# Kernel tuning notes

Hardware: AMD Instinct MI355X
Metric: run time of the kernel (lower is better)

Reference implementation:

```python
import jax, jax.numpy as jnp
import numpy as np

T = 1.0        # temperature t from __init__
THRESH = 0.3   # hard-negative margin from forward
B, D, C, P, N = 64, 256, 100000, 8, 32


def setup_inputs():
    key = jax.random.key(0)
    k1, k2, k3, k4, k5, k6, k7 = jax.random.split(key, 7)
    inputs = jax.random.normal(k1, (B, D), jnp.float32)
    V = jax.random.normal(k2, (C, D), jnp.float32) * 0.05  # memory bank (buffer)
    targets = jax.random.randint(k3, (B,), 0, C)
    pos_idx = jax.random.randint(k4, (B, P), 0, B)
    neg_idx = jax.random.randint(k5, (B, N), 0, B)
    pos_mask = jax.random.randint(k6, (B, P), 0, 2).at[:, 0].set(1)  # >=1 positive
    neg_mask = jax.random.randint(k7, (B, N), 0, 2)
    return {"inputs": inputs, "V": V, "targets": targets,
            "pos_idx": pos_idx, "pos_mask": pos_mask,
            "neg_idx": neg_idx, "neg_mask": neg_mask}


def _forward(inputs, V, targets, pos_idx, pos_mask, neg_idx, neg_mask):
    # Exclusive.forward: inputs @ V.T, scaled by t
    logits = (inputs @ V.T) * T                       # [B, C]
    logp = jax.nn.log_softmax(logits, axis=-1)
    bu_loss = -jnp.mean(jnp.take_along_axis(logp, targets[:, None], axis=1))

    # cosine similarity among batch samples
    nrm = jnp.maximum(jnp.linalg.norm(inputs, axis=1, keepdims=True), 1e-12)
    ni = inputs / nrm
    sim = ni @ ni.T                                   # [B, B]

    rows = jnp.arange(B)[:, None]
    # hardest positive: min similarity over valid positive pairs
    psims = sim[rows, pos_idx]                        # [B, P]
    pm = pos_mask.astype(bool)
    hpsims = jnp.min(jnp.where(pm, psims, jnp.inf), axis=1)   # [B]
    hp_loss = jax.nn.softplus(-hpsims)                # BCE-with-logits vs target 1

    # hard negatives: those with sim > (hardest_pos - 0.3)
    nsims = sim[rows, neg_idx]                        # [B, N]
    sel = neg_mask.astype(bool) & (nsims > (hpsims - THRESH)[:, None])
    cnt = jnp.sum(sel, axis=1)
    hn_sum = jnp.sum(jnp.where(sel, jax.nn.softplus(nsims), 0.0), axis=1)
    hn_loss = jnp.where(cnt > 0, hn_sum / jnp.maximum(cnt, 1), 0.0)

    h_loss = jnp.mean(hp_loss + hn_loss)
    return bu_loss + h_loss, logits


def reference(inputs, V, targets, pos_idx, pos_mask, neg_idx, neg_mask):
    return _forward(inputs, V, targets, pos_idx, pos_mask, neg_idx, neg_mask)
```

## Files before the change

kernel.cpp:

```cpp
#include <hip/hip_runtime.h>
#include <hip/hip_bf16.h>
#include <math.h>

#define B_DIM 64
#define D_DIM 256
#define C_DIM 100000
#define P_DIM 8
#define N_DIM 32
#define BLK_COLS 128
#define GBLK 782
#define NCHUNK 8
#define NBANK 64

typedef __attribute__((ext_vector_type(8))) short bf16x8;
typedef __attribute__((ext_vector_type(16))) float f32x16;

__device__ __forceinline__ unsigned short bf16_rn(float f) {
    unsigned int u = __float_as_uint(f);
    unsigned int r = (u + 0x7FFFu + ((u >> 16) & 1u)) >> 16;
    return (unsigned short)r;
}

__device__ __forceinline__ void split_bf16(float x, unsigned short& hi, unsigned short& lo) {
    unsigned int bx = __float_as_uint(x);
    unsigned int hb = bx & 0xFFFF0000u;
    hi = (unsigned short)(hb >> 16);
    lo = bf16_rn(x - __uint_as_float(hb));
}

__device__ __forceinline__ float softplusf(float x) { return log1pf(expf(x)); }

__device__ __forceinline__ short f2bf(float x) {
    __hip_bfloat16 b = __float2bfloat16(x);
    return *reinterpret_cast<short*>(&b);
}

__device__ __forceinline__ void async_copy16(const float* src, float* lds_base) {
    __builtin_amdgcn_global_load_lds(
        (const __attribute__((address_space(1))) unsigned int*)src,
        (__attribute__((address_space(3))) unsigned int*)lds_base,
        16, 0, 0);
}

__global__ __launch_bounds__(512)
void prep_kernel(const float* __restrict__ X,
                 const int* __restrict__ pos_idx, const int* __restrict__ pos_mask,
                 const int* __restrict__ neg_idx, const int* __restrict__ neg_mask,
                 float* __restrict__ wsH, unsigned short* __restrict__ wsA,
                 float* __restrict__ wsQ, float* __restrict__ wsT) {
    __shared__ unsigned short fHi[2048 * 8];
    __shared__ unsigned short fLo[2048 * 8];
    __shared__ float sim[64][64];
    __shared__ float inv[64];
    __shared__ float hp[64];
    __shared__ float contrib[64];
    const int tid = threadIdx.x;
    for (int i = tid; i < NBANK * 64; i += 512) wsQ[i] = 0.0f;
    if (tid < 64) wsT[tid] = 0.0f;
    if (tid < 256) {
        int r = tid >> 2, q = tid & 3;
        const float* row = X + r * D_DIM + q * 64;
        float s = 0.0f;
        #pragma unroll
        for (int i = 0; i < 64; i += 4) {
            float4 v = *(const float4*)(row + i);
            s += v.x * v.x + v.y * v.y + v.z * v.z + v.w * v.w;
        }
        s += __shfl_xor(s, 1);
        s += __shfl_xor(s, 2);
        if (q == 0) inv[r] = 1.0f / fmaxf(sqrtf(s), 1e-12f);
    }
    __syncthreads();
    for (int t = tid; t < 2048; t += 512) {
        int l = t & 63, kg = (t >> 6) & 15, mt = t >> 10;
        int row = mt * 32 + (l & 31);
        int col0 = kg * 16 + 8 * (l >> 5);
        const float* src = X + row * D_DIM + col0;
        float iv = inv[row];
        #pragma unroll
        for (int j = 0; j < 8; ++j) {
            unsigned short h, lo;
            split_bf16(src[j] * iv, h, lo);
            fHi[t * 8 + j] = h;
            fLo[t * 8 + j] = lo;
            wsA[t * 8 + j] = (unsigned short)f2bf(src[j]);
        }
    }
    __syncthreads();
    if ((tid >> 6) < 4) {
        int w = tid >> 6, l = tid & 63;
        int mt = w >> 1, nt = w & 1;
        f32x16 acc;
        #pragma unroll
        for (int i = 0; i < 16; ++i) acc[i] = 0.0f;
        #pragma unroll
        for (int ks = 0; ks < 16; ++ks) {
            const bf16x8 ah = *(const bf16x8*)&fHi[((mt * 16 + ks) * 64 + l) * 8];
            const bf16x8 al = *(const bf16x8*)&fLo[((mt * 16 + ks) * 64 + l) * 8];
            const bf16x8 bh = *(const bf16x8*)&fHi[((nt * 16 + ks) * 64 + l) * 8];
            const bf16x8 bl = *(const bf16x8*)&fLo[((nt * 16 + ks) * 64 + l) * 8];
            acc = __builtin_amdgcn_mfma_f32_32x32x16_bf16(ah, bh, acc, 0, 0, 0);
            acc = __builtin_amdgcn_mfma_f32_32x32x16_bf16(al, bh, acc, 0, 0, 0);
            acc = __builtin_amdgcn_mfma_f32_32x32x16_bf16(ah, bl, acc, 0, 0, 0);
        }
        #pragma unroll
        for (int r = 0; r < 16; ++r) {
            int brow = mt * 32 + (r & 3) + 8 * (r >> 2) + 4 * (l >> 5);
            int bcol = nt * 32 + (l & 31);
            sim[brow][bcol] = acc[r];
        }
    }
    __syncthreads();
    if (tid < 256) {
        int r = tid >> 2, q = tid & 3;
        const float INF = __int_as_float(0x7f800000);
        float m = INF;
        #pragma unroll
        for (int pp = 0; pp < 2; ++pp) {
            int p = q * 2 + pp;
            int j = pos_idx[r * P_DIM + p];
            int msk = pos_mask[r * P_DIM + p];
            float ps = sim[r][j];
            m = fminf(m, msk ? ps : INF);
        }
        m = fminf(m, __shfl_xor(m, 1));
        m = fminf(m, __shfl_xor(m, 2));
        if (q == 0) hp[r] = m;
    }
    __syncthreads();
    if (tid < 256) {
        int r = tid >> 2, q = tid & 3;
        float thr = hp[r] - 0.3f;
        float sum = 0.0f; int cnt = 0;
        #pragma unroll
        for (int nn = 0; nn < 8; ++nn) {
            int n = q * 8 + nn;
            int j = neg_idx[r * N_DIM + n];
            int msk = neg_mask[r * N_DIM + n];
            float ns = sim[r][j];
            if (msk && (ns > thr)) { cnt += 1; sum += softplusf(ns); }
        }
        sum += __shfl_xor(sum, 1); cnt += __shfl_xor(cnt, 1);
        sum += __shfl_xor(sum, 2); cnt += __shfl_xor(cnt, 2);
        if (q == 0) {
            float hn = (cnt > 0) ? (sum / (float)cnt) : 0.0f;
            contrib[r] = softplusf(-hp[r]) + hn;
        }
    }
    __syncthreads();
    if (tid == 0) {
        float s = 0.0f;
        for (int i = 0; i < 64; ++i) s += contrib[i];
        wsH[0] = s * (1.0f / 64.0f);
    }
}

__global__ __launch_bounds__(256)
void logits_kernel(const float* __restrict__ V, const unsigned short* __restrict__ wsA,
                   const int* __restrict__ targets, float* __restrict__ out,
                   float* __restrict__ wsQ, float* __restrict__ wsT) {
    __shared__ float shm[12288];
    __shared__ int tgt[64];
    const int tid = threadIdx.x;
    const int w = tid >> 6, l = tid & 63;
    const int c0 = blockIdx.x * BLK_COLS;
    const int hi = l >> 5;
    if (tid < 64) tgt[tid] = targets[tid];

    #define STAGE(kc, b)                                                        \
        {                                                                       \
            _Pragma("unroll")                                                   \
            for (int j = 0; j < 4; ++j) {                                       \
                int U = (j * 4 + w) * 64 + l;                                   \
                int colL = U >> 3, up = U & 7;                                  \
                int us = up ^ (colL & 7);                                       \
                int cc = c0 + colL; cc = (cc < C_DIM) ? cc : (C_DIM - 1);       \
                const float* src = V + (size_t)cc * D_DIM + (kc) * 32 + us * 4; \
                async_copy16(src, &shm[(b) * 4096 + (j * 4 + w) * 256]);        \
            }                                                                   \
        }

    STAGE(0, 0);
    STAGE(1, 1);

    f32x16 acc0, acc1;
    #pragma unroll
    for (int i = 0; i < 16; ++i) { acc0[i] = 0.0f; acc1[i] = 0.0f; }

    const int colL = w * 32 + (l & 31);
    const int cbase = colL * 32;
    const int cm7 = colL & 7;

    #pragma unroll
    for (int kc = 0; kc < NCHUNK; ++kc) {
        if (kc < NCHUNK - 1) asm volatile("s_waitcnt vmcnt(4)" ::: "memory");
        else                 asm volatile("s_waitcnt vmcnt(0)" ::: "memory");
        __builtin_amdgcn_s_barrier();
        const float* vb = &shm[(kc % 3) * 4096];
        #pragma unroll
        for (int h = 0; h < 2; ++h) {
            const int kg = kc * 2 + h;
            const bf16x8 a0 = *(const bf16x8*)(wsA + ((0 * 16 + kg) * 64 + l) * 8);
            const bf16x8 a1 = *(const bf16x8*)(wsA + ((1 * 16 + kg) * 64 + l) * 8);
            const int u0 = h * 4 + 2 * hi;
            float4 v0 = *(const float4*)&vb[cbase + ((u0    ) ^ cm7) * 4];
            float4 v1 = *(const float4*)&vb[cbase + ((u0 + 1) ^ cm7) * 4];
            bf16x8 vh;
            vh[0] = f2bf(v0.x); vh[1] = f2bf(v0.y); vh[2] = f2bf(v0.z); vh[3] = f2bf(v0.w);
            vh[4] = f2bf(v1.x); vh[5] = f2bf(v1.y); vh[6] = f2bf(v1.z); vh[7] = f2bf(v1.w);
            acc0 = __builtin_amdgcn_mfma_f32_32x32x16_bf16(vh, a0, acc0, 0, 0, 0);
            acc1 = __builtin_amdgcn_mfma_f32_32x32x16_bf16(vh, a1, acc1, 0, 0, 0);
        }
        if (kc < NCHUNK - 2) STAGE(kc + 2, (kc + 2) % 3);
    }
    #undef STAGE
    __syncthreads();

    float* ldsT = &shm[w * 2112];
    float* sred = &shm[8448];
    const int b0 = l & 31, b1 = 32 + (l & 31);
    const int tb0 = tgt[b0], tb1 = tgt[b1];
    float s0 = 0.0f, s1 = 0.0f;
    #pragma unroll
    for (int r = 0; r < 16; ++r) {
        const int cl = (r & 3) + 8 * (r >> 2) + 4 * hi;
        const int c = c0 + w * 32 + cl;
        const float v0 = acc0[r], v1 = acc1[r];
        ldsT[b0 * 33 + cl] = v0;
        ldsT[b1 * 33 + cl] = v1;
        if (c < C_DIM) {
            s0 += expf(v0);
            s1 += expf(v1);
            if (c == tb0) atomicAdd(&wsT[b0], v0);
            if (c == tb1) atomicAdd(&wsT[b1], v1);
        }
    }
    s0 += __shfl_xor(s0, 32);
    s1 += __shfl_xor(s1, 32);
    if (l < 32) { sred[w * 64 + l] = s0; sred[w * 64 + 32 + l] = s1; }
    __syncthreads();
    if (tid < 64) {
        float s = (sred[tid] + sred[64 + tid]) + (sred[128 + tid] + sred[192 + tid]);
        atomicAdd(&wsQ[(blockIdx.x & (NBANK - 1)) * 64 + tid], s);
    }
    const int cg = c0 + w * 32 + (l & 31);
    if (cg < C_DIM) {
        #pragma unroll
        for (int rr = 0; rr < 32; ++rr) {
            const int b = 2 * rr + hi;
            out[1 + (size_t)b * C_DIM + cg] = ldsT[b * 33 + (l & 31)];
        }
    }
}

__global__ __launch_bounds__(64)
void final_kernel(float* __restrict__ out, const float* __restrict__ wsQ,
                  const float* __restrict__ wsT, const float* __restrict__ wsH) {
    int b = threadIdx.x;
    float S = 0.0f;
    #pragma unroll
    for (int k = 0; k < NBANK; ++k) S += wsQ[k * 64 + b];
    float lb = logf(S) - wsT[b];
    #pragma unroll
    for (int m = 1; m <= 32; m <<= 1) lb += __shfl_xor(lb, m);
    if (b == 0) out[0] = lb * (1.0f / 64.0f) + wsH[0];
}

extern "C" void kernel_launch(void* const* d_in, const int* in_sizes, int n_in,
                              void* d_out, int out_size, void* d_ws, size_t ws_size,
                              hipStream_t stream) {
    (void)in_sizes; (void)n_in; (void)out_size; (void)ws_size;
    const float* X        = (const float*)d_in[0];
    const float* V        = (const float*)d_in[1];
    const int*   targets  = (const int*)d_in[2];
    const int*   pos_idx  = (const int*)d_in[3];
    const int*   pos_mask = (const int*)d_in[4];
    const int*   neg_idx  = (const int*)d_in[5];
    const int*   neg_mask = (const int*)d_in[6];
    float* out = (float*)d_out;
    float*          wsH = (float*)d_ws;
    float*          wsQ = (float*)d_ws + 64;
    float*          wsT = (float*)d_ws + 64 + NBANK * 64;
    unsigned short* wsA = (unsigned short*)((char*)d_ws + 32768);

    hipLaunchKernelGGL(prep_kernel, dim3(1), dim3(512), 0, stream,
                       X, pos_idx, pos_mask, neg_idx, neg_mask, wsH, wsA, wsQ, wsT);
    hipLaunchKernelGGL(logits_kernel, dim3(GBLK), dim3(256), 0, stream,
                       V, wsA, targets, out, wsQ, wsT);
    hipLaunchKernelGGL(final_kernel, dim3(1), dim3(64), 0, stream, out, wsQ, wsT, wsH);
}
```

Measured before the change: 53.48 us.

## Fold similarity loss into logits grid and finalize via last-block counter

Replaces the single-block prep kernel with a small parallel bf16 fragment-packing kernel. The cosine-similarity hard-mining loss now runs in an extra block of the logits grid, computing only the needed dot products directly in fp32. The separate final kernel is removed: the last block to finish, detected with an atomic counter, reduces the softmax sums. The logits pipeline also moves to 16-wide K chunks with prefetched A fragments, smaller LDS stages and fewer reduction banks. This saves launch overhead and the serial prep latency, at the cost of fence/atomic completion logic and more barriers per tile.

```diff
diff --git a/kernel.cpp b/kernel.cpp
--- a/kernel.cpp
+++ b/kernel.cpp
@@ -8,25 +8,13 @@
 #define P_DIM 8
 #define N_DIM 32
 #define BLK_COLS 128
-#define GBLK 782
-#define NCHUNK 8
-#define NBANK 64
+#define GTILES 782
+#define GRID_TOT (GTILES + 1)
+#define NCHUNK 16
+#define NBANK 32
 
 typedef __attribute__((ext_vector_type(8))) short bf16x8;
 typedef __attribute__((ext_vector_type(16))) float f32x16;
-
-__device__ __forceinline__ unsigned short bf16_rn(float f) {
-    unsigned int u = __float_as_uint(f);
-    unsigned int r = (u + 0x7FFFu + ((u >> 16) & 1u)) >> 16;
-    return (unsigned short)r;
-}
-
-__device__ __forceinline__ void split_bf16(float x, unsigned short& hi, unsigned short& lo) {
-    unsigned int bx = __float_as_uint(x);
-    unsigned int hb = bx & 0xFFFF0000u;
-    hi = (unsigned short)(hb >> 16);
-    lo = bf16_rn(x - __uint_as_float(hb));
-}
 
 __device__ __forceinline__ float softplusf(float x) { return log1pf(expf(x)); }
 
@@ -42,228 +30,218 @@
         16, 0, 0);
 }
 
-__global__ __launch_bounds__(512)
-void prep_kernel(const float* __restrict__ X,
-                 const int* __restrict__ pos_idx, const int* __restrict__ pos_mask,
-                 const int* __restrict__ neg_idx, const int* __restrict__ neg_mask,
-                 float* __restrict__ wsH, unsigned short* __restrict__ wsA,
-                 float* __restrict__ wsQ, float* __restrict__ wsT) {
-    __shared__ unsigned short fHi[2048 * 8];
-    __shared__ unsigned short fLo[2048 * 8];
-    __shared__ float sim[64][64];
-    __shared__ float inv[64];
-    __shared__ float hp[64];
-    __shared__ float contrib[64];
-    const int tid = threadIdx.x;
-    for (int i = tid; i < NBANK * 64; i += 512) wsQ[i] = 0.0f;
-    if (tid < 64) wsT[tid] = 0.0f;
-    if (tid < 256) {
-        int r = tid >> 2, q = tid & 3;
-        const float* row = X + r * D_DIM + q * 64;
-        float s = 0.0f;
-        #pragma unroll
-        for (int i = 0; i < 64; i += 4) {
-            float4 v = *(const float4*)(row + i);
-            s += v.x * v.x + v.y * v.y + v.z * v.z + v.w * v.w;
-        }
-        s += __shfl_xor(s, 1);
-        s += __shfl_xor(s, 2);
-        if (q == 0) inv[r] = 1.0f / fmaxf(sqrtf(s), 1e-12f);
-    }
-    __syncthreads();
-    for (int t = tid; t < 2048; t += 512) {
-        int l = t & 63, kg = (t >> 6) & 15, mt = t >> 10;
-        int row = mt * 32 + (l & 31);
-        int col0 = kg * 16 + 8 * (l >> 5);
-        const float* src = X + row * D_DIM + col0;
-        float iv = inv[row];
-        #pragma unroll
-        for (int j = 0; j < 8; ++j) {
-            unsigned short h, lo;
-            split_bf16(src[j] * iv, h, lo);
-            fHi[t * 8 + j] = h;
-            fLo[t * 8 + j] = lo;
-            wsA[t * 8 + j] = (unsigned short)f2bf(src[j]);
-        }
-    }
-    __syncthreads();
-    if ((tid >> 6) < 4) {
-        int w = tid >> 6, l = tid & 63;
-        int mt = w >> 1, nt = w & 1;
-        f32x16 acc;
-        #pragma unroll
-        for (int i = 0; i < 16; ++i) acc[i] = 0.0f;
-        #pragma unroll
-        for (int ks = 0; ks < 16; ++ks) {
-            const bf16x8 ah = *(const bf16x8*)&fHi[((mt * 16 + ks) * 64 + l) * 8];
-            const bf16x8 al = *(const bf16x8*)&fLo[((mt * 16 + ks) * 64 + l) * 8];
-            const bf16x8 bh = *(const bf16x8*)&fHi[((nt * 16 + ks) * 64 + l) * 8];
-            const bf16x8 bl = *(const bf16x8*)&fLo[((nt * 16 + ks) * 64 + l) * 8];
-            acc = __builtin_amdgcn_mfma_f32_32x32x16_bf16(ah, bh, acc, 0, 0, 0);
-            acc = __builtin_amdgcn_mfma_f32_32x32x16_bf16(al, bh, acc, 0, 0, 0);
-            acc = __builtin_amdgcn_mfma_f32_32x32x16_bf16(ah, bl, acc, 0, 0, 0);
-        }
-        #pragma unroll
-        for (int r = 0; r < 16; ++r) {
-            int brow = mt * 32 + (r & 3) + 8 * (r >> 2) + 4 * (l >> 5);
-            int bcol = nt * 32 + (l & 31);
-            sim[brow][bcol] = acc[r];
-        }
-    }
-    __syncthreads();
-    if (tid < 256) {
-        int r = tid >> 2, q = tid & 3;
-        const float INF = __int_as_float(0x7f800000);
-        float m = INF;
-        #pragma unroll
-        for (int pp = 0; pp < 2; ++pp) {
-            int p = q * 2 + pp;
-            int j = pos_idx[r * P_DIM + p];
-            int msk = pos_mask[r * P_DIM + p];
-            float ps = sim[r][j];
-            m = fminf(m, msk ? ps : INF);
-        }
-        m = fminf(m, __shfl_xor(m, 1));
-        m = fminf(m, __shfl_xor(m, 2));
-        if (q == 0) hp[r] = m;
-    }
-    __syncthreads();
-    if (tid < 256) {
-        int r = tid >> 2, q = tid & 3;
-        float thr = hp[r] - 0.3f;
-        float sum = 0.0f; int cnt = 0;
-        #pragma unroll
-        for (int nn = 0; nn < 8; ++nn) {
-            int n = q * 8 + nn;
-            int j = neg_idx[r * N_DIM + n];
-            int msk = neg_mask[r * N_DIM + n];
-            float ns = sim[r][j];
-            if (msk && (ns > thr)) { cnt += 1; sum += softplusf(ns); }
-        }
-        sum += __shfl_xor(sum, 1); cnt += __shfl_xor(cnt, 1);
-        sum += __shfl_xor(sum, 2); cnt += __shfl_xor(cnt, 2);
-        if (q == 0) {
-            float hn = (cnt > 0) ? (sum / (float)cnt) : 0.0f;
-            contrib[r] = softplusf(-hp[r]) + hn;
-        }
-    }
-    __syncthreads();
-    if (tid == 0) {
-        float s = 0.0f;
-        for (int i = 0; i < 64; ++i) s += contrib[i];
-        wsH[0] = s * (1.0f / 64.0f);
-    }
+__device__ __forceinline__ float dot256(const float* __restrict__ a, const float* __restrict__ b) {
+    float sx = 0.f, sy = 0.f, sz = 0.f, sw = 0.f;
+    #pragma unroll 8
+    for (int i = 0; i < D_DIM; i += 4) {
+        float4 va = *(const float4*)(a + i);
+        float4 vb = *(const float4*)(b + i);
+        sx += va.x * vb.x; sy += va.y * vb.y;
+        sz += va.z * vb.z; sw += va.w * vb.w;
+    }
+    return (sx + sy) + (sz + sw);
 }
 
 __global__ __launch_bounds__(256)
-void logits_kernel(const float* __restrict__ V, const unsigned short* __restrict__ wsA,
-                   const int* __restrict__ targets, float* __restrict__ out,
-                   float* __restrict__ wsQ, float* __restrict__ wsT) {
-    __shared__ float shm[12288];
-    __shared__ int tgt[64];
+void frag_kernel(const float* __restrict__ X, unsigned short* __restrict__ wsA,
+                 float* __restrict__ wsQ, float* __restrict__ wsT,
+                 unsigned int* __restrict__ wsC) {
+    const int t = blockIdx.x * 256 + threadIdx.x;
+    const int l = t & 63, kg = (t >> 6) & 15, mt = t >> 10;
+    const int row = mt * 32 + (l & 31);
+    const int col0 = kg * 16 + 8 * (l >> 5);
+    const float* src = X + row * D_DIM + col0;
+    float4 v0 = *(const float4*)src;
+    float4 v1 = *(const float4*)(src + 4);
+    bf16x8 h;
+    h[0] = f2bf(v0.x); h[1] = f2bf(v0.y); h[2] = f2bf(v0.z); h[3] = f2bf(v0.w);
+    h[4] = f2bf(v1.x); h[5] = f2bf(v1.y); h[6] = f2bf(v1.z); h[7] = f2bf(v1.w);
+    *(bf16x8*)(wsA + t * 8) = h;
+    if (blockIdx.x == 0) {
+        for (int i = threadIdx.x; i < NBANK * 64; i += 256) wsQ[i] = 0.f;
+        if (threadIdx.x < 64) wsT[threadIdx.x] = 0.f;
+        if (threadIdx.x == 0) wsC[0] = 0u;
+    }
+}
+
+__global__ __launch_bounds__(256)
+void logits_kernel(const float* __restrict__ V, const float* __restrict__ X,
+                   const unsigned short* __restrict__ wsA,
+                   const int* __restrict__ targets,
+                   const int* __restrict__ pos_idx, const int* __restrict__ pos_mask,
+                   const int* __restrict__ neg_idx, const int* __restrict__ neg_mask,
+                   float* __restrict__ out,
+                   float* __restrict__ wsQ, float* __restrict__ wsT,
+                   float* __restrict__ wsH, unsigned int* __restrict__ wsC) {
+    __shared__ float shm[8704];
     const int tid = threadIdx.x;
     const int w = tid >> 6, l = tid & 63;
-    const int c0 = blockIdx.x * BLK_COLS;
     const int hi = l >> 5;
-    if (tid < 64) tgt[tid] = targets[tid];
-
-    #define STAGE(kc, b)                                                        \
-        {                                                                       \
-            _Pragma("unroll")                                                   \
-            for (int j = 0; j < 4; ++j) {                                       \
-                int U = (j * 4 + w) * 64 + l;                                   \
-                int colL = U >> 3, up = U & 7;                                  \
-                int us = up ^ (colL & 7);                                       \
-                int cc = c0 + colL; cc = (cc < C_DIM) ? cc : (C_DIM - 1);       \
-                const float* src = V + (size_t)cc * D_DIM + (kc) * 32 + us * 4; \
-                async_copy16(src, &shm[(b) * 4096 + (j * 4 + w) * 256]);        \
-            }                                                                   \
-        }
-
-    STAGE(0, 0);
-    STAGE(1, 1);
-
-    f32x16 acc0, acc1;
-    #pragma unroll
-    for (int i = 0; i < 16; ++i) { acc0[i] = 0.0f; acc1[i] = 0.0f; }
-
-    const int colL = w * 32 + (l & 31);
-    const int cbase = colL * 32;
-    const int cm7 = colL & 7;
-
-    #pragma unroll
-    for (int kc = 0; kc < NCHUNK; ++kc) {
-        if (kc < NCHUNK - 1) asm volatile("s_waitcnt vmcnt(4)" ::: "memory");
-        else                 asm volatile("s_waitcnt vmcnt(0)" ::: "memory");
-        __builtin_amdgcn_s_barrier();
-        const float* vb = &shm[(kc % 3) * 4096];
-        #pragma unroll
-        for (int h = 0; h < 2; ++h) {
-            const int kg = kc * 2 + h;
-            const bf16x8 a0 = *(const bf16x8*)(wsA + ((0 * 16 + kg) * 64 + l) * 8);
-            const bf16x8 a1 = *(const bf16x8*)(wsA + ((1 * 16 + kg) * 64 + l) * 8);
-            const int u0 = h * 4 + 2 * hi;
-            float4 v0 = *(const float4*)&vb[cbase + ((u0    ) ^ cm7) * 4];
-            float4 v1 = *(const float4*)&vb[cbase + ((u0 + 1) ^ cm7) * 4];
+
+    if (blockIdx.x < GTILES) {
+        const int c0 = blockIdx.x * BLK_COLS;
+
+        #define STAGE(kc, b)                                                        \
+            {                                                                       \
+                _Pragma("unroll")                                                   \
+                for (int j = 0; j < 2; ++j) {                                       \
+                    int U = (j * 4 + w) * 64 + l;                                   \
+                    int colL = U >> 2, up = U & 3;                                  \
+                    int us = up ^ ((colL >> 1) & 3);                                \
+                    int cc = c0 + colL; cc = (cc < C_DIM) ? cc : (C_DIM - 1);       \
+                    const float* src = V + (size_t)cc * D_DIM + (kc) * 16 + us * 4; \
+                    async_copy16(src, &shm[(b) * 2048 + (j * 4 + w) * 256]);        \
+                }                                                                   \
+            }
+        #define AFETCH(kc, s)                                                       \
+            {                                                                       \
+                frg[s][0] = *(const bf16x8*)(wsA + (((kc)     ) * 64 + l) * 8);     \
+                frg[s][1] = *(const bf16x8*)(wsA + (((kc) + 16) * 64 + l) * 8);     \
+            }
+
+        bf16x8 frg[2][2];
+        AFETCH(0, 0);
+        STAGE(0, 0);
+        STAGE(1, 1);
+
+        f32x16 acc0, acc1;
+        #pragma unroll
+        for (int i = 0; i < 16; ++i) { acc0[i] = 0.0f; acc1[i] = 0.0f; }
+
+        const int colL = w * 32 + (l & 31);
+        const int cbase = colL * 16;
+        const int cm = (colL >> 1) & 3;
+
+        #pragma unroll
+        for (int kc = 0; kc < NCHUNK; ++kc) {
+            if (kc < NCHUNK - 1) asm volatile("s_waitcnt vmcnt(2)" ::: "memory");
+            else                 asm volatile("s_waitcnt vmcnt(0)" ::: "memory");
+            __builtin_amdgcn_s_barrier();
+            asm volatile("" ::: "memory");
+            __builtin_amdgcn_sched_barrier(0);
+            if (kc < NCHUNK - 1) AFETCH(kc + 1, (kc + 1) & 1);
+            if (kc < NCHUNK - 2) STAGE(kc + 2, (kc + 2) % 3);
+            const float* vb = &shm[(kc % 3) * 2048];
+            const int u0 = 2 * hi;
+            float4 v0 = *(const float4*)&vb[cbase + ((u0    ) ^ cm) * 4];
+            float4 v1 = *(const float4*)&vb[cbase + ((u0 + 1) ^ cm) * 4];
             bf16x8 vh;
             vh[0] = f2bf(v0.x); vh[1] = f2bf(v0.y); vh[2] = f2bf(v0.z); vh[3] = f2bf(v0.w);
             vh[4] = f2bf(v1.x); vh[5] = f2bf(v1.y); vh[6] = f2bf(v1.z); vh[7] = f2bf(v1.w);
+            const bf16x8 a0 = frg[kc & 1][0], a1 = frg[kc & 1][1];
             acc0 = __builtin_amdgcn_mfma_f32_32x32x16_bf16(vh, a0, acc0, 0, 0, 0);
             acc1 = __builtin_amdgcn_mfma_f32_32x32x16_bf16(vh, a1, acc1, 0, 0, 0);
         }
-        if (kc < NCHUNK - 2) STAGE(kc + 2, (kc + 2) % 3);
-    }
-    #undef STAGE
+        #undef STAGE
+        #undef AFETCH
+        __syncthreads();
+
+        float* ldsT = &shm[w * 2112];
+        float* sred = &shm[8448];
+        const int b0 = l & 31, b1 = 32 + (l & 31);
+        const int tb0 = targets[b0], tb1 = targets[b1];
+        float s0 = 0.0f, s1 = 0.0f;
+        #pragma unroll
+        for (int r = 0; r < 16; ++r) {
+            const int cl = (r & 3) + 8 * (r >> 2) + 4 * hi;
+            const int c = c0 + w * 32 + cl;
+            const float v0 = acc0[r], v1 = acc1[r];
+            ldsT[b0 * 33 + cl] = v0;
+            ldsT[b1 * 33 + cl] = v1;
+            if (c < C_DIM) {
+                s0 += expf(v0);
+                s1 += expf(v1);
+                if (c == tb0) atomicAdd(&wsT[b0], v0);
+                if (c == tb1) atomicAdd(&wsT[b1], v1);
+            }
+        }
+        s0 += __shfl_xor(s0, 32);
+        s1 += __shfl_xor(s1, 32);
+        if (l < 32) { sred[w * 64 + l] = s0; sred[w * 64 + 32 + l] = s1; }
+        __syncthreads();
+        if (tid < 64) {
+            float s = (sred[tid] + sred[64 + tid]) + (sred[128 + tid] + sred[192 + tid]);
+            atomicAdd(&wsQ[(blockIdx.x & (NBANK - 1)) * 64 + tid], s);
+        }
+        const int cg = c0 + w * 32 + (l & 31);
+        if (cg < C_DIM) {
+            #pragma unroll
+            for (int rr = 0; rr < 32; ++rr) {
+                const int b = 2 * rr + hi;
+                out[1 + (size_t)b * C_DIM + cg] = ldsT[b * 33 + (l & 31)];
+            }
+        }
+    } else {
+        float* inv = shm;
+        float* contrib = shm + 64;
+        const int r = tid >> 2, q = tid & 3;
+        {
+            const float* row = X + r * D_DIM + q * 64;
+            float s = 0.0f;
+            #pragma unroll
+            for (int i = 0; i < 64; i += 4) {
+                float4 v = *(const float4*)(row + i);
+                s += v.x * v.x + v.y * v.y + v.z * v.z + v.w * v.w;
+            }
+            s += __shfl_xor(s, 1);
+            s += __shfl_xor(s, 2);
+            if (q == 0) inv[r] = 1.0f / fmaxf(sqrtf(s), 1e-12f);
+        }
+        __syncthreads();
+        const float* Ar = X + r * D_DIM;
+        const float ir = inv[r];
+        const float INF = __int_as_float(0x7f800000);
+        float m = INF;
+        #pragma unroll
+        for (int pp = 0; pp < 2; ++pp) {
+            int p = q * 2 + pp;
+            if (pos_mask[r * P_DIM + p]) {
+                int j = pos_idx[r * P_DIM + p];
+                float d = dot256(Ar, X + j * D_DIM) * ir * inv[j];
+                m = fminf(m, d);
+            }
+        }
+        m = fminf(m, __shfl_xor(m, 1));
+        m = fminf(m, __shfl_xor(m, 2));
+        const float thr = m - 0.3f;
+        float sum = 0.0f; int cnt = 0;
+        #pragma unroll 2
+        for (int nn = 0; nn < 8; ++nn) {
+            int n = q * 8 + nn;
+            if (neg_mask[r * N_DIM + n]) {
+                int j = neg_idx[r * N_DIM + n];
+                float d = dot256(Ar, X + j * D_DIM) * ir * inv[j];
+                if (d > thr) { cnt += 1; sum += softplusf(d); }
+            }
+        }
+        sum += __shfl_xor(sum, 1); cnt += __shfl_xor(cnt, 1);
+        sum += __shfl_xor(sum, 2); cnt += __shfl_xor(cnt, 2);
+        if (q == 0) contrib[r] = softplusf(-m) + ((cnt > 0) ? sum / (float)cnt : 0.0f);
+        __syncthreads();
+        if (tid == 0) {
+            float s = 0.0f;
+            for (int i = 0; i < 64; ++i) s += contrib[i];
+            wsH[0] = s * (1.0f / 64.0f);
+        }
+    }
+
     __syncthreads();
-
-    float* ldsT = &shm[w * 2112];
-    float* sred = &shm[8448];
-    const int b0 = l & 31, b1 = 32 + (l & 31);
-    const int tb0 = tgt[b0], tb1 = tgt[b1];
-    float s0 = 0.0f, s1 = 0.0f;
-    #pragma unroll
-    for (int r = 0; r < 16; ++r) {
-        const int cl = (r & 3) + 8 * (r >> 2) + 4 * hi;
-        const int c = c0 + w * 32 + cl;
-        const float v0 = acc0[r], v1 = acc1[r];
-        ldsT[b0 * 33 + cl] = v0;
-        ldsT[b1 * 33 + cl] = v1;
-        if (c < C_DIM) {
-            s0 += expf(v0);
-            s1 += expf(v1);
-            if (c == tb0) atomicAdd(&wsT[b0], v0);
-            if (c == tb1) atomicAdd(&wsT[b1], v1);
-        }
-    }
-    s0 += __shfl_xor(s0, 32);
-    s1 += __shfl_xor(s1, 32);
-    if (l < 32) { sred[w * 64 + l] = s0; sred[w * 64 + 32 + l] = s1; }
+    __threadfence();
+    if (tid == 0) {
+        unsigned int old = atomicAdd(wsC, 1u);
+        ((int*)shm)[0] = (old == (unsigned int)(GRID_TOT - 1)) ? 1 : 0;
+    }
     __syncthreads();
-    if (tid < 64) {
-        float s = (sred[tid] + sred[64 + tid]) + (sred[128 + tid] + sred[192 + tid]);
-        atomicAdd(&wsQ[(blockIdx.x & (NBANK - 1)) * 64 + tid], s);
-    }
-    const int cg = c0 + w * 32 + (l & 31);
-    if (cg < C_DIM) {
-        #pragma unroll
-        for (int rr = 0; rr < 32; ++rr) {
-            const int b = 2 * rr + hi;
-            out[1 + (size_t)b * C_DIM + cg] = ldsT[b * 33 + (l & 31)];
-        }
-    }
-}
-
-__global__ __launch_bounds__(64)
-void final_kernel(float* __restrict__ out, const float* __restrict__ wsQ,
-                  const float* __restrict__ wsT, const float* __restrict__ wsH) {
-    int b = threadIdx.x;
-    float S = 0.0f;
-    #pragma unroll
-    for (int k = 0; k < NBANK; ++k) S += wsQ[k * 64 + b];
-    float lb = logf(S) - wsT[b];
-    #pragma unroll
-    for (int m = 1; m <= 32; m <<= 1) lb += __shfl_xor(lb, m);
-    if (b == 0) out[0] = lb * (1.0f / 64.0f) + wsH[0];
+    if (((int*)shm)[0] && tid < 64) {
+        float S = 0.0f;
+        #pragma unroll
+        for (int k = 0; k < NBANK; ++k) S += atomicAdd(&wsQ[k * 64 + tid], 0.0f);
+        float T = atomicAdd(&wsT[tid], 0.0f);
+        float lb = logf(S) - T;
+        #pragma unroll
+        for (int m = 1; m <= 32; m <<= 1) lb += __shfl_xor(lb, m);
+        if (tid == 0) out[0] = lb * (1.0f / 64.0f) + atomicAdd(&wsH[0], 0.0f);
+    }
 }
 
 extern "C" void kernel_launch(void* const* d_in, const int* in_sizes, int n_in,
@@ -281,11 +259,11 @@
     float*          wsH = (float*)d_ws;
     float*          wsQ = (float*)d_ws + 64;
     float*          wsT = (float*)d_ws + 64 + NBANK * 64;
+    unsigned int*   wsC = (unsigned int*)((float*)d_ws + 64 + NBANK * 64 + 64);
     unsigned short* wsA = (unsigned short*)((char*)d_ws + 32768);
 
-    hipLaunchKernelGGL(prep_kernel, dim3(1), dim3(512), 0, stream,
-                       X, pos_idx, pos_mask, neg_idx, neg_mask, wsH, wsA, wsQ, wsT);
-    hipLaunchKernelGGL(logits_kernel, dim3(GBLK), dim3(256), 0, stream,
-                       V, wsA, targets, out, wsQ, wsT);
-    hipLaunchKernelGGL(final_kernel, dim3(1), dim3(64), 0, stream, out, wsQ, wsT, wsH);
-}
+    hipLaunchKernelGGL(frag_kernel, dim3(8), dim3(256), 0, stream, X, wsA, wsQ, wsT, wsC);
+    hipLaunchKernelGGL(logits_kernel, dim3(GRID_TOT), dim3(256), 0, stream,
+                       V, X, wsA, targets, pos_idx, pos_mask, neg_idx, neg_mask,
+                       out, wsQ, wsT, wsH, wsC);
+}
```

Result: slower. 191.1 us (+257.3%).
